# Performance work log

Hardware: AMD Instinct MI355X
Metric: run time of the kernel (lower is better)

The kernel has to match this reference:

```python
import jax, jax.numpy as jnp
import numpy as np

B, S, D, H, NB = 512, 200, 256, 4, 2
DH = D // H
N_ITEMS = 100001  # item_num + 1 (padding idx 0)
EPS = 1e-8


def _ln(x, g, b):
    m = x.mean(-1, keepdims=True)
    v = ((x - m) ** 2).mean(-1, keepdims=True)
    return (x - m) / jnp.sqrt(v + EPS) * g + b


def setup_inputs() -> dict:
    key = jax.random.key(0)
    ks = jax.random.split(key, 20)
    f32 = jnp.float32
    item_emb = jax.random.normal(ks[0], (N_ITEMS, D), f32) * 0.02
    item_emb = item_emb.at[0].set(0.0)  # padding_idx=0
    pos_emb = jax.random.normal(ks[1], (S, D), f32) * 0.02
    inp = {
        'item_emb': item_emb,
        'pos_emb': pos_emb,
        'ln1_g': jnp.ones((NB, D), f32),
        'ln1_b': jnp.zeros((NB, D), f32),
        'in_w': jax.random.normal(ks[2], (NB, 3 * D, D), f32) * 0.02,
        'in_b': jnp.zeros((NB, 3 * D), f32),
        'out_w': jax.random.normal(ks[3], (NB, D, D), f32) * 0.02,
        'out_b': jnp.zeros((NB, D), f32),
        'ln2_g': jnp.ones((NB, D), f32),
        'ln2_b': jnp.zeros((NB, D), f32),
        'c1_w': jax.random.normal(ks[4], (NB, D, D), f32) * 0.02,
        'c1_b': jnp.zeros((NB, D), f32),
        'c2_w': jax.random.normal(ks[5], (NB, D, D), f32) * 0.02,
        'c2_b': jnp.zeros((NB, D), f32),
        'last_g': jnp.ones((D,), f32),
        'last_b': jnp.zeros((D,), f32),
        'user_ids': jax.random.randint(ks[6], (B,), 0, 10000),
        'log_seqs': jax.random.randint(ks[7], (B, S), 0, N_ITEMS),
        'pos_seqs': jax.random.randint(ks[8], (B, S), 0, N_ITEMS),
        'neg_seqs': jax.random.randint(ks[9], (B, S), 0, N_ITEMS),
    }
    return inp


def reference(item_emb, pos_emb, ln1_g, ln1_b, in_w, in_b, out_w, out_b,
              ln2_g, ln2_b, c1_w, c1_b, c2_w, c2_b, last_g, last_b,
              user_ids, log_seqs, pos_seqs, neg_seqs):
    seqs = item_emb[log_seqs] * jnp.asarray(D ** 0.5, item_emb.dtype)
    seqs = seqs + pos_emb[None, :, :]  # positions = arange(S)
    tl_mask = (log_seqs != 0)[..., None].astype(seqs.dtype)  # [B,S,1]
    seqs = seqs * tl_mask
    causal = jnp.tril(jnp.ones((S, S), bool))  # True = attend
    scale = 1.0 / np.sqrt(DH)
    for i in range(NB):
        Q = _ln(seqs, ln1_g[i], ln1_b[i])
        q = (Q @ in_w[i, :D].T + in_b[i, :D]).reshape(B, S, H, DH)
        k = (seqs @ in_w[i, D:2 * D].T + in_b[i, D:2 * D]).reshape(B, S, H, DH)
        v = (seqs @ in_w[i, 2 * D:].T + in_b[i, 2 * D:]).reshape(B, S, H, DH)
        scores = jnp.einsum('bqhd,bkhd->bhqk', q, k) * scale
        scores = jnp.where(causal[None, None], scores, -jnp.inf)
        attn = jax.nn.softmax(scores, axis=-1)
        o = jnp.einsum('bhqk,bkhd->bqhd', attn, v).reshape(B, S, D)
        o = o @ out_w[i].T + out_b[i]
        seqs = Q + o  # residual is on layernormed Q (as in source)
        seqs = _ln(seqs, ln2_g[i], ln2_b[i])
        h1 = jax.nn.relu(seqs @ c1_w[i].T + c1_b[i])
        seqs = (h1 @ c2_w[i].T + c2_b[i] + seqs) * tl_mask
    log_feats = _ln(seqs, last_g, last_b)
    pos_embs = item_emb[pos_seqs]
    neg_embs = item_emb[neg_seqs]
    pos_logits = (log_feats * pos_embs).sum(-1)
    neg_logits = (log_feats * neg_embs).sum(-1)
    return (pos_logits, neg_logits)
```

## Files before the change

### kernel.cpp

```cpp
#include <hip/hip_runtime.h>
#include <math.h>

namespace {

constexpr int kB = 512, kS = 200, kD = 256, kH = 4;
constexpr int kM = kB * kS;
constexpr float kEps = 1e-8f;

typedef short bf16x8 __attribute__((ext_vector_type(8)));
typedef float f32x4 __attribute__((ext_vector_type(4)));

__device__ __forceinline__ float bf2f(unsigned short s) {
  return __uint_as_float(((unsigned)s) << 16);
}
__device__ __forceinline__ unsigned cvtpk(float lo, float hi) {
  unsigned r;
  asm("v_cvt_pk_bf16_f32 %0, %1, %2" : "=v"(r) : "v"(lo), "v"(hi));
  return r;
}
__device__ __forceinline__ void gload16(const void* g, void* l) {
  __builtin_amdgcn_global_load_lds(
      (const __attribute__((address_space(1))) void*)g,
      (__attribute__((address_space(3))) void*)l, 16, 0, 0);
}
__device__ __forceinline__ void vm3() { asm volatile("s_waitcnt vmcnt(3)" ::: "memory"); }
__device__ __forceinline__ void vm0() { asm volatile("s_waitcnt vmcnt(0)" ::: "memory"); }
__device__ __forceinline__ void lk0() { asm volatile("s_waitcnt lgkmcnt(0)" ::: "memory"); }
__device__ __forceinline__ void bar() { asm volatile("s_barrier" ::: "memory"); }

__global__ __launch_bounds__(256) void cvt4_kernel(
    const float* __restrict__ w0, const float* __restrict__ w1,
    const float* __restrict__ w2, const float* __restrict__ w3,
    const float* __restrict__ ln1g,
    unsigned short* __restrict__ o0, unsigned short* __restrict__ o1,
    unsigned short* __restrict__ o2, unsigned short* __restrict__ o3) {
  int blk = blockIdx.x;
  const float* src;
  unsigned short* dst;
  int base;
  bool isin = false;
  if (blk < 384)      { src = w0; dst = o0; base = blk; isin = true; }
  else if (blk < 512) { src = w1; dst = o1; base = blk - 384; }
  else if (blk < 640) { src = w2; dst = o2; base = blk - 512; }
  else                { src = w3; dst = o3; base = blk - 640; }
  int i4 = (base * 256 + threadIdx.x) * 4;
  float4 v = *reinterpret_cast<const float4*>(src + i4);
  if (isin) {
    int layer = (i4 >= 196608) ? 1 : 0;
    int rem = i4 - layer * 196608;
    int n = rem >> 8;
    int k = rem & 255;
    if (n < 256) {
      float4 g = *reinterpret_cast<const float4*>(ln1g + layer * 256 + k);
      v.x *= g.x; v.y *= g.y; v.z *= g.z; v.w *= g.w;
    }
  }
  uint2 o = {cvtpk(v.x, v.y), cvtpk(v.z, v.w)};
  *reinterpret_cast<uint2*>(dst + i4) = o;
}

__global__ __launch_bounds__(64) void s1s2_kernel(
    const float* __restrict__ in_w, const float* __restrict__ in_b,
    const float* __restrict__ ln1g, const float* __restrict__ ln1b,
    float* __restrict__ s1o, float* __restrict__ s2o) {
  int blk = blockIdx.x;
  int layer = blk >> 8, n = blk & 255;
  int k = threadIdx.x * 4;
  float4 w = *reinterpret_cast<const float4*>(in_w + (size_t)layer * 196608 + n * 256 + k);
  float4 g = *reinterpret_cast<const float4*>(ln1g + layer * 256 + k);
  float4 b = *reinterpret_cast<const float4*>(ln1b + layer * 256 + k);
  float a = w.x * g.x + w.y * g.y + w.z * g.z + w.w * g.w;
  float c = w.x * b.x + w.y * b.y + w.z * b.z + w.w * b.w;
#pragma unroll
  for (int o = 32; o >= 1; o >>= 1) { a += __shfl_xor(a, o); c += __shfl_xor(c, o); }
  if (threadIdx.x == 0) {
    s1o[blk] = a;
    s2o[blk] = c + in_b[layer * 768 + n];
  }
}

__global__ __launch_bounds__(512) void embed_kernel(
    const float* __restrict__ item_emb, const float* __restrict__ pos_emb,
    const int* __restrict__ log_seqs, unsigned short* __restrict__ x,
    float2* __restrict__ stats) {
  int bs = blockIdx.x * 8 + (threadIdx.x >> 6);
  int s = bs % kS;
  int idx = log_seqs[bs];
  float msk = (idx != 0) ? 1.f : 0.f;
  int t = threadIdx.x & 63;
  float4 a = reinterpret_cast<const float4*>(item_emb + (size_t)idx * kD)[t];
  float4 p = reinterpret_cast<const float4*>(pos_emb + (size_t)s * kD)[t];
  float v[4];
  v[0] = (a.x * 16.f + p.x) * msk;
  v[1] = (a.y * 16.f + p.y) * msk;
  v[2] = (a.z * 16.f + p.z) * msk;
  v[3] = (a.w * 16.f + p.w) * msk;
  uint2 r = {cvtpk(v[0], v[1]), cvtpk(v[2], v[3])};
  reinterpret_cast<uint2*>(x + (size_t)bs * kD)[t] = r;
  float sm = v[0] + v[1] + v[2] + v[3];
#pragma unroll
  for (int o = 32; o >= 1; o >>= 1) sm += __shfl_xor(sm, o);
  float mean = sm * (1.f / kD);
  float d0 = v[0] - mean, d1 = v[1] - mean, d2 = v[2] - mean, d3 = v[3] - mean;
  float vs = d0 * d0 + d1 * d1 + d2 * d2 + d3 * d3;
#pragma unroll
  for (int o = 32; o >= 1; o >>= 1) vs += __shfl_xor(vs, o);
  if (t == 0) stats[bs] = {mean, rsqrtf(vs * (1.f / kD) + kEps)};
}

template <int MODE, int LN, int G3>
__global__ __launch_bounds__(512, 4) void gemm2(
    const unsigned short* __restrict__ A, int lda,
    const unsigned short* __restrict__ W,
    const float* __restrict__ bias,
    const unsigned short* __restrict__ R, int ldr,
    const int* __restrict__ logseq,
    const float* __restrict__ lng, const float* __restrict__ lnb,
    const float* __restrict__ qg, const float* __restrict__ qb,
    const float2* __restrict__ statsIn, float2* __restrict__ statsOut,
    const float* __restrict__ s1v, const float* __restrict__ s2v,
    const float* __restrict__ iembf, const int* __restrict__ posq,
    const int* __restrict__ negq, float* __restrict__ outlg,
    unsigned short* __restrict__ C, int ldc) {
  __shared__ __attribute__((aligned(16))) unsigned short SMEM[36864];
  __shared__ float red1[128][4];
  __shared__ float red2[128][4];
  const int tid = threadIdx.x, lane = tid & 63, wid = tid >> 6;
  int m0, n0;
  if (G3) {
    int g = blockIdx.x / 24, sub = blockIdx.x % 24;
    m0 = (g * 8 + (sub & 7)) * 128;
    n0 = (sub >> 3) * 256;
  } else {
    m0 = blockIdx.x * 128;
    n0 = 0;
  }
  const int wm = wid >> 2, wn = wid & 3;
  const int lrow = lane & 15, kgrp = lane >> 4;
  const int srow = tid >> 2;
  const int sslot = (tid & 3) ^ (srow & 3);
  const unsigned short* gA  = A + (size_t)(m0 + srow) * lda + sslot * 8;
  const unsigned short* gW0 = W + (size_t)(n0 + srow) * kD + sslot * 8;
  const unsigned short* gW1 = gW0 + (size_t)128 * kD;
  const int sa = (kgrp ^ (lrow & 3)) * 8;

#define STAGE(kk, bb)                                                   \
  do {                                                                  \
    gload16(gA + (kk) * 32, &SMEM[(bb) * 4096 + wid * 512]);            \
    gload16(gW0 + (kk) * 32, &SMEM[12288 + (bb) * 8192 + wid * 512]);   \
    gload16(gW1 + (kk) * 32, &SMEM[16384 + (bb) * 8192 + wid * 512]);   \
  } while (0)

  f32x4 acc[4][4] = {};
  STAGE(0, 0);
  STAGE(1, 1);
#pragma unroll
  for (int k = 0; k < 8; ++k) {
    if (k < 7) vm3(); else vm0();
    bar();
    const int buf = k % 3;
    bf16x8 af[4], bfr[4];
#pragma unroll
    for (int x = 0; x < 4; ++x) {
      af[x]  = *reinterpret_cast<const bf16x8*>(
          &SMEM[12288 + buf * 8192 + (wn * 64 + x * 16 + lrow) * 32 + sa]);
      bfr[x] = *reinterpret_cast<const bf16x8*>(
          &SMEM[buf * 4096 + (wm * 64 + x * 16 + lrow) * 32 + sa]);
    }
    if (k + 2 < 8) STAGE(k + 2, (k + 2) % 3);
    __builtin_amdgcn_s_setprio(1);
#pragma unroll
    for (int na = 0; na < 4; ++na)
#pragma unroll
      for (int mb = 0; mb < 4; ++mb)
        acc[na][mb] = __builtin_amdgcn_mfma_f32_16x16x32_bf16(
            af[na], bfr[mb], acc[na][mb], 0, 0, 0);
    __builtin_amdgcn_s_setprio(0);
  }
#undef STAGE
  __syncthreads();
  const bool qpath = (MODE == 4) && (n0 == 0);
  float msk[4];
  float2 st[4];
  if (MODE == 3 || MODE == 6) {
#pragma unroll
    for (int mb = 0; mb < 4; ++mb)
      msk[mb] = (logseq[m0 + wm * 64 + mb * 16 + lrow] != 0) ? 1.f : 0.f;
  }
  if (MODE == 5 || (MODE == 4 && n0 == 0)) {
#pragma unroll
    for (int mb = 0; mb < 4; ++mb)
      st[mb] = statsIn[m0 + wm * 64 + mb * 16 + lrow];
  }

  auto computeX = [&](int na, int mb, float x[4]) {
    const int gcol = n0 + wn * 64 + na * 16 + kgrp * 4;
    const f32x4 v = acc[na][mb];
    if (MODE == 4 && qpath) {
      float4 t1 = *reinterpret_cast<const float4*>(s1v + gcol);
      float4 t2 = *reinterpret_cast<const float4*>(s2v + gcol);
      const float s1f[4] = {t1.x, t1.y, t1.z, t1.w};
      const float s2f[4] = {t2.x, t2.y, t2.z, t2.w};
#pragma unroll
      for (int r = 0; r < 4; ++r)
        x[r] = st[mb].y * (v[r] - st[mb].x * s1f[r]) + s2f[r];
      return;
    }
    float4 b4 = *reinterpret_cast<const float4*>(bias + gcol);
    const float bx[4] = {b4.x, b4.y, b4.z, b4.w};
    if (MODE == 1) {
#pragma unroll
      for (int r = 0; r < 4; ++r) x[r] = fmaxf(v[r] + bx[r], 0.f);
    } else if (MODE == 4) {
#pragma unroll
      for (int r = 0; r < 4; ++r) x[r] = v[r] + bx[r];
    } else if (MODE == 3 || MODE == 6) {
      int m = m0 + wm * 64 + mb * 16 + lrow;
      ushort4 rv = *reinterpret_cast<const ushort4*>(R + (size_t)m * ldr + gcol);
      const unsigned short* rs = reinterpret_cast<const unsigned short*>(&rv);
#pragma unroll
      for (int r = 0; r < 4; ++r)
        x[r] = (v[r] + bx[r] + bf2f(rs[r])) * msk[mb];
    } else {
      int m = m0 + wm * 64 + mb * 16 + lrow;
      ushort4 rv = *reinterpret_cast<const ushort4*>(R + (size_t)m * ldr + gcol);
      const unsigned short* rs = reinterpret_cast<const unsigned short*>(&rv);
      float4 t1 = *reinterpret_cast<const float4*>(qg + gcol);
      float4 t2 = *reinterpret_cast<const float4*>(qb + gcol);
      const float g4[4] = {t1.x, t1.y, t1.z, t1.w};
      const float qb4[4] = {t2.x, t2.y, t2.z, t2.w};
#pragma unroll
      for (int r = 0; r < 4; ++r) {
        float q = (bf2f(rs[r]) - st[mb].x) * st[mb].y * g4[r] + qb4[r];
        x[r] = v[r] + bx[r] + q;
      }
    }
  };

  if (MODE == 6) {
    float* SL = reinterpret_cast<float*>(SMEM);
    int pi[4], ni[4];
#pragma unroll
    for (int mb = 0; mb < 4; ++mb) {
      int m = m0 + wm * 64 + mb * 16 + lrow;
      pi[mb] = posq[m];
      ni[mb] = negq[m];
    }
#pragma unroll
    for (int mb = 0; mb < 4; ++mb) {
      float4 peL[4], neL[4];
#pragma unroll
      for (int na = 0; na < 4; ++na) {
        int gcol = n0 + wn * 64 + na * 16 + kgrp * 4;
        peL[na] = *reinterpret_cast<const float4*>(iembf + (size_t)pi[mb] * 256 + gcol);
        neL[na] = *reinterpret_cast<const float4*>(iembf + (size_t)ni[mb] * 256 + gcol);
      }
      float sa_ = 0.f, sb_ = 0.f;
      float s1p = 0.f, s2p = 0.f, s3p = 0.f;
      float s1n = 0.f, s2n = 0.f, s3n = 0.f;
#pragma unroll
      for (int na = 0; na < 4; ++na) {
        float x[4];
        computeX(na, mb, x);
        int gcol = n0 + wn * 64 + na * 16 + kgrp * 4;
        float4 g4v = *reinterpret_cast<const float4*>(lng + gcol);
        float4 b4v = *reinterpret_cast<const float4*>(lnb + gcol);
        const float gg[4] = {g4v.x, g4v.y, g4v.z, g4v.w};
        const float lb[4] = {b4v.x, b4v.y, b4v.z, b4v.w};
        const float pef[4] = {peL[na].x, peL[na].y, peL[na].z, peL[na].w};
        const float nef[4] = {neL[na].x, neL[na].y, neL[na].z, neL[na].w};
#pragma unroll
        for (int r = 0; r < 4; ++r) {
          sa_ += x[r];
          sb_ += x[r] * x[r];
          float gp = gg[r] * pef[r], gn = gg[r] * nef[r];
          s1p += x[r] * gp; s2p += gp; s3p += lb[r] * pef[r];
          s1n += x[r] * gn; s2n += gn; s3n += lb[r] * nef[r];
        }
      }
      float vals[8] = {sa_, sb_, s1p, s2p, s3p, s1n, s2n, s3n};
#pragma unroll
      for (int j = 0; j < 8; ++j) {
        vals[j] += __shfl_xor(vals[j], 16);
        vals[j] += __shfl_xor(vals[j], 32);
      }
      if (kgrp == 0) {
        int rl = wm * 64 + mb * 16 + lrow;
        float* dst = &SL[rl * 33 + wn * 8];
#pragma unroll
        for (int j = 0; j < 8; ++j) dst[j] = vals[j];
      }
    }
    __syncthreads();
    if (tid < 128) {
      float t[8] = {0.f, 0.f, 0.f, 0.f, 0.f, 0.f, 0.f, 0.f};
#pragma unroll
      for (int w = 0; w < 4; ++w) {
        const float* src = &SL[tid * 33 + w * 8];
#pragma unroll
        for (int j = 0; j < 8; ++j) t[j] += src[j];
      }
      float mean = t[0] * (1.f / 256.f);
      float var = t[1] * (1.f / 256.f) - mean * mean;
      float inv = rsqrtf(fmaxf(var, 0.f) + kEps);
      int m = m0 + tid;
      outlg[m] = inv * (t[2] - mean * t[3]) + t[4];
      outlg[(size_t)kM + m] = inv * (t[5] - mean * t[6]) + t[7];
    }
    return;
  }

  float mean[4], inv[4];
  if (LN) {
    float sA[4] = {0.f, 0.f, 0.f, 0.f}, sB[4] = {0.f, 0.f, 0.f, 0.f};
#pragma unroll
    for (int na = 0; na < 4; ++na)
#pragma unroll
      for (int mb = 0; mb < 4; ++mb) {
        float x[4];
        computeX(na, mb, x);
#pragma unroll
        for (int r = 0; r < 4; ++r) { sA[mb] += x[r]; sB[mb] += x[r] * x[r]; }
      }
#pragma unroll
    for (int mb = 0; mb < 4; ++mb) {
      sA[mb] += __shfl_xor(sA[mb], 16); sA[mb] += __shfl_xor(sA[mb], 32);
      sB[mb] += __shfl_xor(sB[mb], 16); sB[mb] += __shfl_xor(sB[mb], 32);
    }
    if (kgrp == 0) {
#pragma unroll
      for (int mb = 0; mb < 4; ++mb) {
        int rl = wm * 64 + mb * 16 + lrow;
        red1[rl][wn] = sA[mb];
        red2[rl][wn] = sB[mb];
      }
    }
    __syncthreads();
#pragma unroll
    for (int mb = 0; mb < 4; ++mb) {
      int rl = wm * 64 + mb * 16 + lrow;
      float4 p1 = *reinterpret_cast<const float4*>(red1[rl]);
      float4 p2 = *reinterpret_cast<const float4*>(red2[rl]);
      float t1 = p1.x + p1.y + p1.z + p1.w;
      float t2 = p2.x + p2.y + p2.z + p2.w;
      float mu = t1 * (1.f / 256.f);
      float var = t2 * (1.f / 256.f) - mu * mu;
      mean[mb] = mu;
      inv[mb] = rsqrtf(fmaxf(var, 0.f) + kEps);
    }
    if (LN == 3 && wn == 0 && kgrp == 0) {
#pragma unroll
      for (int mb = 0; mb < 4; ++mb)
        statsOut[m0 + wm * 64 + mb * 16 + lrow] = {mean[mb], inv[mb]};
    }
  }

  unsigned short* eb = &SMEM[wid * 3072];
  const int rr = lane >> 2, c8 = (lane & 3) * 8;
#pragma unroll
  for (int hh = 0; hh < 2; ++hh) {
    lk0();
#pragma unroll
    for (int mbl = 0; mbl < 2; ++mbl) {
      int mb = hh * 2 + mbl;
#pragma unroll
      for (int na = 0; na < 4; ++na) {
        float x[4];
        computeX(na, mb, x);
        if (LN == 1) {
          int gcol = n0 + wn * 64 + na * 16 + kgrp * 4;
          float4 g4v = *reinterpret_cast<const float4*>(lng + gcol);
          float4 b4v = *reinterpret_cast<const float4*>(lnb + gcol);
          x[0] = (x[0] - mean[mb]) * inv[mb] * g4v.x + b4v.x;
          x[1] = (x[1] - mean[mb]) * inv[mb] * g4v.y + b4v.y;
          x[2] = (x[2] - mean[mb]) * inv[mb] * g4v.z + b4v.z;
          x[3] = (x[3] - mean[mb]) * inv[mb] * g4v.w + b4v.w;
        }
        uint2 o = {cvtpk(x[0], x[1]), cvtpk(x[2], x[3])};
        *reinterpret_cast<uint2*>(&eb[(mbl * 16 + lrow) * 72 + na * 16 + kgrp * 4]) = o;
      }
    }
    lk0();
#pragma unroll
    for (int rh = 0; rh < 2; ++rh) {
      int row = rh * 16 + rr;
      uint4 d0 = *reinterpret_cast<const uint4*>(&eb[row * 72 + c8]);
      uint4 d1 = *reinterpret_cast<const uint4*>(&eb[row * 72 + 32 + c8]);
      size_t gbase = (size_t)(m0 + wm * 64 + hh * 32 + row) * ldc + (n0 + wn * 64 + c8);
      *reinterpret_cast<uint4*>(C + gbase) = d0;
      *reinterpret_cast<uint4*>(C + gbase + 32) = d1;
    }
  }
}

__global__ __launch_bounds__(512) void attn_mfma(unsigned short* __restrict__ qkv) {
  constexpr int kVS = 232, kQS = 768;
  __shared__ __attribute__((aligned(16))) unsigned short Kl[200 * 64];
  __shared__ __attribute__((aligned(16))) unsigned short Vt[64 * kVS];
  __shared__ __attribute__((aligned(16))) unsigned short Pt[8 * 636];
  int b = blockIdx.x >> 2, h = blockIdx.x & 3;
  int tid = threadIdx.x, lane = tid & 63, wid = tid >> 6;
  const unsigned short* kvb = qkv + (size_t)b * kS * kQS + 256 + h * 64;
  for (int i = tid; i < 1600; i += 512) {
    int row = i >> 3, slot = i & 7;
    *reinterpret_cast<uint4*>(&Kl[row * 64 + ((slot ^ (row & 7)) << 3)]) =
        *reinterpret_cast<const uint4*>(kvb + (size_t)row * kQS + slot * 8);
  }
  for (int i = tid; i < 3200; i += 512) {
    int row = i >> 4, d0 = (i & 15) * 4;
    ushort4 v = *reinterpret_cast<const ushort4*>(kvb + 256 + (size_t)row * kQS + d0);
    Vt[(d0 + 0) * kVS + row] = v.x;
    Vt[(d0 + 1) * kVS + row] = v.y;
    Vt[(d0 + 2) * kVS + row] = v.z;
    Vt[(d0 + 3) * kVS + row] = v.w;
  }
  for (int i = tid; i < 2048; i += 512) {
    int d = i >> 5, c = i & 31;
    Vt[d * kVS + 200 + c] = 0;
  }
  __syncthreads();

  int qcol = lane & 15, kgrp = lane >> 4;
  const float scale2 = 0.18033688f;
  int packed = (wid < 3) ? (0xFFFC - wid) : (0xFF09 + (wid - 3) * 15);
  unsigned short* ptw = &Pt[wid * 636];
#pragma unroll
  for (int ti = 0; ti < 2; ++ti) {
    int t = (packed >> (ti * 4)) & 15;
    if (t == 15) break;
    int qb = t * 16;
    int qrow = qb + qcol;
    int qm = min(qrow, kS - 1);
    const unsigned short* qrp = qkv + (size_t)(b * kS + qm) * kQS + h * 64;
    bf16x8 qf0 = *reinterpret_cast<const bf16x8*>(qrp + kgrp * 8);
    bf16x8 qf1 = *reinterpret_cast<const bf16x8*>(qrp + 32 + kgrp * 8);
    f32x4 accO[4] = {};
    float l_run = 0.f;
    int nc = (qb + 47) >> 5;
    for (int c = 0; c < nc; ++c) {
      int kbase = c * 32;
      f32x4 s0 = {}, s1 = {};
      int kr0 = min(kbase + qcol, kS - 1);
      int kr1 = min(kbase + 16 + qcol, kS - 1);
      const unsigned short* K0a = &Kl[kr0 * 64 + ((kgrp ^ (kr0 & 7)) << 3)];
      const unsigned short* K0b = &Kl[kr0 * 64 + (((kgrp + 4) ^ (kr0 & 7)) << 3)];
      const unsigned short* K1a = &Kl[kr1 * 64 + ((kgrp ^ (kr1 & 7)) << 3)];
      const unsigned short* K1b = &Kl[kr1 * 64 + (((kgrp + 4) ^ (kr1 & 7)) << 3)];
      s0 = __builtin_amdgcn_mfma_f32_16x16x32_bf16(*reinterpret_cast<const bf16x8*>(K0a), qf0, s0, 0, 0, 0);
      s0 = __builtin_amdgcn_mfma_f32_16x16x32_bf16(*reinterpret_cast<const bf16x8*>(K0b), qf1, s0, 0, 0, 0);
      s1 = __builtin_amdgcn_mfma_f32_16x16x32_bf16(*reinterpret_cast<const bf16x8*>(K1a), qf0, s1, 0, 0, 0);
      s1 = __builtin_amdgcn_mfma_f32_16x16x32_bf16(*reinterpret_cast<const bf16x8*>(K1b), qf1, s1, 0, 0, 0);
      float p[8];
      float psum = 0.f;
#pragma unroll
      for (int r = 0; r < 4; ++r) {
        int key0 = kbase + kgrp * 4 + r;
        int key1 = key0 + 16;
        float x0 = (key0 <= qm) ? fmaf(s0[r], scale2, -8.f) : -3.0e38f;
        float x1 = (key1 <= qm) ? fmaf(s1[r], scale2, -8.f) : -3.0e38f;
        p[r] = exp2f(x0);
        p[r + 4] = exp2f(x1);
        psum += p[r] + p[r + 4];
      }
      l_run += psum;
      uint2 w0 = {cvtpk(p[0], p[1]), cvtpk(p[2], p[3])};
      uint2 w1 = {cvtpk(p[4], p[5]), cvtpk(p[6], p[7])};
      *reinterpret_cast<uint2*>(&ptw[qcol * 40 + kgrp * 4]) = w0;
      *reinterpret_cast<uint2*>(&ptw[qcol * 40 + 16 + kgrp * 4]) = w1;
      bf16x8 pf = *reinterpret_cast<const bf16x8*>(&ptw[qcol * 40 + kgrp * 8]);
#pragma unroll
      for (int nf = 0; nf < 4; ++nf) {
        bf16x8 vf = *reinterpret_cast<const bf16x8*>(
            &Vt[(nf * 16 + qcol) * kVS + kbase + kgrp * 8]);
        accO[nf] = __builtin_amdgcn_mfma_f32_16x16x32_bf16(vf, pf, accO[nf], 0, 0, 0);
      }
    }
    float l_tot = l_run;
    l_tot += __shfl_xor(l_tot, 16);
    l_tot += __shfl_xor(l_tot, 32);
    float inv = 1.f / l_tot;
    if (qrow < kS) {
      unsigned short* op = qkv + (size_t)(b * kS + qrow) * kQS + h * 64;
#pragma unroll
      for (int nf = 0; nf < 4; ++nf) {
        uint2 o4 = {cvtpk(accO[nf][0] * inv, accO[nf][1] * inv),
                    cvtpk(accO[nf][2] * inv, accO[nf][3] * inv)};
        *reinterpret_cast<uint2*>(op + nf * 16 + kgrp * 4) = o4;
      }
    }
  }
}

}

extern "C" void kernel_launch(void* const* d_in, const int* in_sizes, int n_in,
                              void* d_out, int out_size, void* d_ws,
                              size_t ws_size, hipStream_t stream) {
  const float* item_emb = (const float*)d_in[0];
  const float* pos_emb  = (const float*)d_in[1];
  const float* ln1_g = (const float*)d_in[2];
  const float* ln1_b = (const float*)d_in[3];
  const float* in_w  = (const float*)d_in[4];
  const float* in_b  = (const float*)d_in[5];
  const float* out_w = (const float*)d_in[6];
  const float* out_b = (const float*)d_in[7];
  const float* ln2_g = (const float*)d_in[8];
  const float* ln2_b = (const float*)d_in[9];
  const float* c1_w  = (const float*)d_in[10];
  const float* c1_b  = (const float*)d_in[11];
  const float* c2_w  = (const float*)d_in[12];
  const float* c2_b  = (const float*)d_in[13];
  const float* last_g = (const float*)d_in[14];
  const float* last_b = (const float*)d_in[15];
  const int* log_seqs = (const int*)d_in[17];
  const int* pos_seqs = (const int*)d_in[18];
  const int* neg_seqs = (const int*)d_in[19];
  float* out = (float*)d_out;

  size_t unit = (size_t)kM * kD;
  unsigned short* X   = (unsigned short*)d_ws;
  unsigned short* QKV = X + unit;
  unsigned short* inw_bf  = X + 4 * unit;
  unsigned short* outw_bf = inw_bf + 2 * 768 * 256;
  unsigned short* c1w_bf  = outw_bf + 2 * 256 * 256;
  unsigned short* c2w_bf  = c1w_bf + 2 * 256 * 256;
  float2* stats = (float2*)(c2w_bf + 2 * 256 * 256);
  float* s1buf = (float*)(stats + 2 * kM);
  float* s2buf = s1buf + 512;

  cvt4_kernel<<<768, 256, 0, stream>>>(in_w, out_w, c1_w, c2_w, ln1_g,
                                       inw_bf, outw_bf, c1w_bf, c2w_bf);
  s1s2_kernel<<<512, 64, 0, stream>>>(in_w, in_b, ln1_g, ln1_b, s1buf, s2buf);
  embed_kernel<<<kM / 8, 512, 0, stream>>>(item_emb, pos_emb, log_seqs, X, stats);

  dim3 g1(kM / 128, 1);
  for (int l = 0; l < 2; ++l) {
    const unsigned short* iw = inw_bf + (size_t)l * 768 * 256;
    float2* stl = stats + (size_t)l * kM;
    gemm2<4, 0, 1><<<kM / 128 * 3, 512, 0, stream>>>(
        X, 256, iw, in_b + l * 768, nullptr, 0, nullptr,
        nullptr, nullptr, nullptr, nullptr, stl, nullptr,
        s1buf + l * 256, s2buf + l * 256, nullptr, nullptr, nullptr, nullptr,
        QKV, 768);
    attn_mfma<<<kB * kH, 512, 0, stream>>>(QKV);
    gemm2<5, 1, 0><<<g1, 512, 0, stream>>>(
        QKV, 768, outw_bf + (size_t)l * kD * kD, out_b + l * kD, X, 256, nullptr,
        ln2_g + l * kD, ln2_b + l * kD, ln1_g + l * kD, ln1_b + l * kD,
        stl, nullptr, nullptr, nullptr, nullptr, nullptr, nullptr, nullptr,
        QKV + 256, 768);
    gemm2<1, 0, 0><<<g1, 512, 0, stream>>>(
        QKV + 256, 768, c1w_bf + (size_t)l * kD * kD, c1_b + l * kD, nullptr, 0,
        nullptr, nullptr, nullptr, nullptr, nullptr, nullptr, nullptr,
        nullptr, nullptr, nullptr, nullptr, nullptr, nullptr, QKV + 512, 768);
    if (l == 0) {
      gemm2<3, 3, 0><<<g1, 512, 0, stream>>>(
          QKV + 512, 768, c2w_bf, c2_b, QKV + 256, 768, log_seqs,
          nullptr, nullptr, nullptr, nullptr, nullptr, stats + kM,
          nullptr, nullptr, nullptr, nullptr, nullptr, nullptr, X, 256);
    } else {
      gemm2<6, 0, 0><<<g1, 512, 0, stream>>>(
          QKV + 512, 768, c2w_bf + (size_t)kD * kD, c2_b + kD, QKV + 256, 768,
          log_seqs, last_g, last_b, nullptr, nullptr, nullptr, nullptr,
          nullptr, nullptr, item_emb, pos_seqs, neg_seqs, out, X, 256);
    }
  }
}
```

Before: 658.9 us.

## Fuse FFN c1 and c2 GEMMs into one kernel keeping hidden in LDS

Replaces the separate c1 (ReLU) GEMM and c2 residual/LN-stats or final-logit GEMM with a single ffn_fused kernel using 64-row tiles. The ReLU hidden activations stay in swizzled shared memory instead of round-tripping through global QKV storage. The kernel double-buffers weight loads, and the epilogues for layer 0 (stats out) and layer 1 (logits) move into it. Smaller tiles and two weight sweeps per block add weight traffic and may lower MFMA efficiency per block.

```diff
diff --git a/kernel.cpp b/kernel.cpp
--- a/kernel.cpp
+++ b/kernel.cpp
@@ -24,6 +24,7 @@
       (__attribute__((address_space(3))) void*)l, 16, 0, 0);
 }
 __device__ __forceinline__ void vm3() { asm volatile("s_waitcnt vmcnt(3)" ::: "memory"); }
+__device__ __forceinline__ void vm2() { asm volatile("s_waitcnt vmcnt(2)" ::: "memory"); }
 __device__ __forceinline__ void vm0() { asm volatile("s_waitcnt vmcnt(0)" ::: "memory"); }
 __device__ __forceinline__ void lk0() { asm volatile("s_waitcnt lgkmcnt(0)" ::: "memory"); }
 __device__ __forceinline__ void bar() { asm volatile("s_barrier" ::: "memory"); }
@@ -114,13 +115,10 @@
     const unsigned short* __restrict__ W,
     const float* __restrict__ bias,
     const unsigned short* __restrict__ R, int ldr,
-    const int* __restrict__ logseq,
     const float* __restrict__ lng, const float* __restrict__ lnb,
     const float* __restrict__ qg, const float* __restrict__ qb,
-    const float2* __restrict__ statsIn, float2* __restrict__ statsOut,
+    const float2* __restrict__ statsIn,
     const float* __restrict__ s1v, const float* __restrict__ s2v,
-    const float* __restrict__ iembf, const int* __restrict__ posq,
-    const int* __restrict__ negq, float* __restrict__ outlg,
     unsigned short* __restrict__ C, int ldc) {
   __shared__ __attribute__((aligned(16))) unsigned short SMEM[36864];
   __shared__ float red1[128][4];
@@ -180,13 +178,7 @@
 #undef STAGE
   __syncthreads();
   const bool qpath = (MODE == 4) && (n0 == 0);
-  float msk[4];
   float2 st[4];
-  if (MODE == 3 || MODE == 6) {
-#pragma unroll
-    for (int mb = 0; mb < 4; ++mb)
-      msk[mb] = (logseq[m0 + wm * 64 + mb * 16 + lrow] != 0) ? 1.f : 0.f;
-  }
   if (MODE == 5 || (MODE == 4 && n0 == 0)) {
 #pragma unroll
     for (int mb = 0; mb < 4; ++mb)
@@ -208,19 +200,9 @@
     }
     float4 b4 = *reinterpret_cast<const float4*>(bias + gcol);
     const float bx[4] = {b4.x, b4.y, b4.z, b4.w};
-    if (MODE == 1) {
-#pragma unroll
-      for (int r = 0; r < 4; ++r) x[r] = fmaxf(v[r] + bx[r], 0.f);
-    } else if (MODE == 4) {
+    if (MODE == 4) {
 #pragma unroll
       for (int r = 0; r < 4; ++r) x[r] = v[r] + bx[r];
-    } else if (MODE == 3 || MODE == 6) {
-      int m = m0 + wm * 64 + mb * 16 + lrow;
-      ushort4 rv = *reinterpret_cast<const ushort4*>(R + (size_t)m * ldr + gcol);
-      const unsigned short* rs = reinterpret_cast<const unsigned short*>(&rv);
-#pragma unroll
-      for (int r = 0; r < 4; ++r)
-        x[r] = (v[r] + bx[r] + bf2f(rs[r])) * msk[mb];
     } else {
       int m = m0 + wm * 64 + mb * 16 + lrow;
       ushort4 rv = *reinterpret_cast<const ushort4*>(R + (size_t)m * ldr + gcol);
@@ -236,79 +218,6 @@
       }
     }
   };
-
-  if (MODE == 6) {
-    float* SL = reinterpret_cast<float*>(SMEM);
-    int pi[4], ni[4];
-#pragma unroll
-    for (int mb = 0; mb < 4; ++mb) {
-      int m = m0 + wm * 64 + mb * 16 + lrow;
-      pi[mb] = posq[m];
-      ni[mb] = negq[m];
-    }
-#pragma unroll
-    for (int mb = 0; mb < 4; ++mb) {
-      float4 peL[4], neL[4];
-#pragma unroll
-      for (int na = 0; na < 4; ++na) {
-        int gcol = n0 + wn * 64 + na * 16 + kgrp * 4;
-        peL[na] = *reinterpret_cast<const float4*>(iembf + (size_t)pi[mb] * 256 + gcol);
-        neL[na] = *reinterpret_cast<const float4*>(iembf + (size_t)ni[mb] * 256 + gcol);
-      }
-      float sa_ = 0.f, sb_ = 0.f;
-      float s1p = 0.f, s2p = 0.f, s3p = 0.f;
-      float s1n = 0.f, s2n = 0.f, s3n = 0.f;
-#pragma unroll
-      for (int na = 0; na < 4; ++na) {
-        float x[4];
-        computeX(na, mb, x);
-        int gcol = n0 + wn * 64 + na * 16 + kgrp * 4;
-        float4 g4v = *reinterpret_cast<const float4*>(lng + gcol);
-        float4 b4v = *reinterpret_cast<const float4*>(lnb + gcol);
-        const float gg[4] = {g4v.x, g4v.y, g4v.z, g4v.w};
-        const float lb[4] = {b4v.x, b4v.y, b4v.z, b4v.w};
-        const float pef[4] = {peL[na].x, peL[na].y, peL[na].z, peL[na].w};
-        const float nef[4] = {neL[na].x, neL[na].y, neL[na].z, neL[na].w};
-#pragma unroll
-        for (int r = 0; r < 4; ++r) {
-          sa_ += x[r];
-          sb_ += x[r] * x[r];
-          float gp = gg[r] * pef[r], gn = gg[r] * nef[r];
-          s1p += x[r] * gp; s2p += gp; s3p += lb[r] * pef[r];
-          s1n += x[r] * gn; s2n += gn; s3n += lb[r] * nef[r];
-        }
-      }
-      float vals[8] = {sa_, sb_, s1p, s2p, s3p, s1n, s2n, s3n};
-#pragma unroll
-      for (int j = 0; j < 8; ++j) {
-        vals[j] += __shfl_xor(vals[j], 16);
-        vals[j] += __shfl_xor(vals[j], 32);
-      }
-      if (kgrp == 0) {
-        int rl = wm * 64 + mb * 16 + lrow;
-        float* dst = &SL[rl * 33 + wn * 8];
-#pragma unroll
-        for (int j = 0; j < 8; ++j) dst[j] = vals[j];
-      }
-    }
-    __syncthreads();
-    if (tid < 128) {
-      float t[8] = {0.f, 0.f, 0.f, 0.f, 0.f, 0.f, 0.f, 0.f};
-#pragma unroll
-      for (int w = 0; w < 4; ++w) {
-        const float* src = &SL[tid * 33 + w * 8];
-#pragma unroll
-        for (int j = 0; j < 8; ++j) t[j] += src[j];
-      }
-      float mean = t[0] * (1.f / 256.f);
-      float var = t[1] * (1.f / 256.f) - mean * mean;
-      float inv = rsqrtf(fmaxf(var, 0.f) + kEps);
-      int m = m0 + tid;
-      outlg[m] = inv * (t[2] - mean * t[3]) + t[4];
-      outlg[(size_t)kM + m] = inv * (t[5] - mean * t[6]) + t[7];
-    }
-    return;
-  }
 
   float mean[4], inv[4];
   if (LN) {
@@ -347,11 +256,6 @@
       float var = t2 * (1.f / 256.f) - mu * mu;
       mean[mb] = mu;
       inv[mb] = rsqrtf(fmaxf(var, 0.f) + kEps);
-    }
-    if (LN == 3 && wn == 0 && kgrp == 0) {
-#pragma unroll
-      for (int mb = 0; mb < 4; ++mb)
-        statsOut[m0 + wm * 64 + mb * 16 + lrow] = {mean[mb], inv[mb]};
     }
   }
 
@@ -390,6 +294,285 @@
       *reinterpret_cast<uint4*>(C + gbase) = d0;
       *reinterpret_cast<uint4*>(C + gbase + 32) = d1;
     }
+  }
+}
+
+template <int LAST>
+__global__ __launch_bounds__(512, 4) void ffn_fused(
+    const unsigned short* __restrict__ A, int lda,
+    const unsigned short* __restrict__ W1, const float* __restrict__ b1,
+    const unsigned short* __restrict__ W2, const float* __restrict__ b2,
+    const int* __restrict__ logseq,
+    const float* __restrict__ lng, const float* __restrict__ lnb,
+    float2* __restrict__ statsOut,
+    const float* __restrict__ iembf, const int* __restrict__ posq,
+    const int* __restrict__ negq, float* __restrict__ outlg,
+    unsigned short* __restrict__ C, int ldc) {
+  __shared__ __attribute__((aligned(16))) unsigned short SMEM[36864];
+  __shared__ float red1[64][4];
+  __shared__ float red2[64][4];
+  const int tid = threadIdx.x, lane = tid & 63, wid = tid >> 6;
+  const int m0 = blockIdx.x * 64;
+  const int wm = wid >> 2, wn = wid & 3;
+  const int lrow = lane & 15, kgrp = lane >> 4;
+  unsigned short* As = SMEM;
+  unsigned short* Ws = SMEM + 4096;
+  unsigned short* H1 = SMEM + 20480;
+  const int arow = (wid & 3) * 16 + (lane >> 2);
+  const int aslot = (lane & 3) ^ (arow & 3);
+  const unsigned short* gA = A + (size_t)(m0 + arow) * lda + aslot * 8;
+  const int wrow0 = wid * 32 + (lane >> 2);
+  const int wrow1 = wrow0 + 16;
+  const int ws0 = (lane & 3) ^ (wrow0 & 3);
+  const int ws1 = (lane & 3) ^ (wrow1 & 3);
+  const unsigned short* gW10 = W1 + wrow0 * 256 + ws0 * 8;
+  const unsigned short* gW11 = W1 + wrow1 * 256 + ws1 * 8;
+  const unsigned short* gW20 = W2 + wrow0 * 256 + ws0 * 8;
+  const unsigned short* gW21 = W2 + wrow1 * 256 + ws1 * 8;
+  const int sa = (kgrp ^ (lrow & 3)) * 8;
+  const f32x4 zero = {0.f, 0.f, 0.f, 0.f};
+
+#define STG1(kk, bb)                                               \
+  do {                                                             \
+    if (wid < 4) gload16(gA + (kk) * 32, &As[(bb) * 2048 + wid * 512]); \
+    gload16(gW10 + (kk) * 32, &Ws[(bb) * 8192 + wid * 1024]);      \
+    gload16(gW11 + (kk) * 32, &Ws[(bb) * 8192 + wid * 1024 + 512]);\
+  } while (0)
+
+  f32x4 acc[4][2] = {};
+  STG1(0, 0);
+  STG1(1, 1);
+#pragma unroll
+  for (int k = 0; k < 8; ++k) {
+    if (k < 7) { if (wid < 4) vm3(); else vm2(); } else vm0();
+    bar();
+    const int buf = k & 1;
+    bf16x8 af[4], bfr[2];
+#pragma unroll
+    for (int x = 0; x < 4; ++x)
+      af[x] = *reinterpret_cast<const bf16x8*>(
+          &Ws[buf * 8192 + (wn * 64 + x * 16 + lrow) * 32 + sa]);
+#pragma unroll
+    for (int mb = 0; mb < 2; ++mb)
+      bfr[mb] = *reinterpret_cast<const bf16x8*>(
+          &As[buf * 2048 + (wm * 32 + mb * 16 + lrow) * 32 + sa]);
+    __builtin_amdgcn_s_setprio(1);
+#pragma unroll
+    for (int na = 0; na < 4; ++na)
+#pragma unroll
+      for (int mb = 0; mb < 2; ++mb)
+        acc[na][mb] = __builtin_amdgcn_mfma_f32_16x16x32_bf16(
+            af[na], bfr[mb], acc[na][mb], 0, 0, 0);
+    __builtin_amdgcn_s_setprio(0);
+    bar();
+    if (k + 2 < 8) STG1(k + 2, k & 1);
+  }
+#undef STG1
+#pragma unroll
+  for (int na = 0; na < 4; ++na) {
+    int c0 = wn * 64 + na * 16 + kgrp * 4;
+    float4 b4 = *reinterpret_cast<const float4*>(b1 + c0);
+#pragma unroll
+    for (int mb = 0; mb < 2; ++mb) {
+      int row = wm * 32 + mb * 16 + lrow;
+      f32x4 v = acc[na][mb];
+      float x0 = fmaxf(v[0] + b4.x, 0.f), x1 = fmaxf(v[1] + b4.y, 0.f);
+      float x2 = fmaxf(v[2] + b4.z, 0.f), x3 = fmaxf(v[3] + b4.w, 0.f);
+      int s = wn * 8 + na * 2 + (kgrp >> 1);
+      int addr = row * 256 + ((s ^ (row & 7)) << 3) + (kgrp & 1) * 4;
+      uint2 o = {cvtpk(x0, x1), cvtpk(x2, x3)};
+      *reinterpret_cast<uint2*>(&H1[addr]) = o;
+    }
+  }
+  __syncthreads();
+#pragma unroll
+  for (int na = 0; na < 4; ++na)
+#pragma unroll
+    for (int mb = 0; mb < 2; ++mb) acc[na][mb] = zero;
+
+#define STG2(kk, bb)                                               \
+  do {                                                             \
+    gload16(gW20 + (kk) * 32, &Ws[(bb) * 8192 + wid * 1024]);      \
+    gload16(gW21 + (kk) * 32, &Ws[(bb) * 8192 + wid * 1024 + 512]);\
+  } while (0)
+
+  STG2(0, 0);
+  STG2(1, 1);
+#pragma unroll
+  for (int k = 0; k < 8; ++k) {
+    if (k < 7) vm2(); else vm0();
+    bar();
+    const int buf = k & 1;
+    bf16x8 af[4], bfr[2];
+#pragma unroll
+    for (int x = 0; x < 4; ++x)
+      af[x] = *reinterpret_cast<const bf16x8*>(
+          &Ws[buf * 8192 + (wn * 64 + x * 16 + lrow) * 32 + sa]);
+#pragma unroll
+    for (int mb = 0; mb < 2; ++mb) {
+      int row = wm * 32 + mb * 16 + lrow;
+      bfr[mb] = *reinterpret_cast<const bf16x8*>(
+          &H1[row * 256 + (((k * 4 + kgrp) ^ (row & 7)) << 3)]);
+    }
+    __builtin_amdgcn_s_setprio(1);
+#pragma unroll
+    for (int na = 0; na < 4; ++na)
+#pragma unroll
+      for (int mb = 0; mb < 2; ++mb)
+        acc[na][mb] = __builtin_amdgcn_mfma_f32_16x16x32_bf16(
+            af[na], bfr[mb], acc[na][mb], 0, 0, 0);
+    __builtin_amdgcn_s_setprio(0);
+    bar();
+    if (k + 2 < 8) STG2(k + 2, k & 1);
+  }
+#undef STG2
+  __syncthreads();
+
+  float msk[2];
+#pragma unroll
+  for (int mb = 0; mb < 2; ++mb)
+    msk[mb] = (logseq[m0 + wm * 32 + mb * 16 + lrow] != 0) ? 1.f : 0.f;
+
+  auto computeY = [&](int na, int mb, float x[4]) {
+    int gcol = wn * 64 + na * 16 + kgrp * 4;
+    int m = m0 + wm * 32 + mb * 16 + lrow;
+    f32x4 v = acc[na][mb];
+    float4 b4 = *reinterpret_cast<const float4*>(b2 + gcol);
+    ushort4 rv = *reinterpret_cast<const ushort4*>(A + (size_t)m * lda + gcol);
+    const unsigned short* rs = reinterpret_cast<const unsigned short*>(&rv);
+    const float bx[4] = {b4.x, b4.y, b4.z, b4.w};
+#pragma unroll
+    for (int r = 0; r < 4; ++r)
+      x[r] = (v[r] + bx[r] + bf2f(rs[r])) * msk[mb];
+  };
+
+  if (LAST == 0) {
+    float sA[2] = {0.f, 0.f}, sB[2] = {0.f, 0.f};
+#pragma unroll
+    for (int na = 0; na < 4; ++na)
+#pragma unroll
+      for (int mb = 0; mb < 2; ++mb) {
+        float x[4];
+        computeY(na, mb, x);
+#pragma unroll
+        for (int r = 0; r < 4; ++r) { sA[mb] += x[r]; sB[mb] += x[r] * x[r]; }
+      }
+#pragma unroll
+    for (int mb = 0; mb < 2; ++mb) {
+      sA[mb] += __shfl_xor(sA[mb], 16); sA[mb] += __shfl_xor(sA[mb], 32);
+      sB[mb] += __shfl_xor(sB[mb], 16); sB[mb] += __shfl_xor(sB[mb], 32);
+    }
+    if (kgrp == 0) {
+#pragma unroll
+      for (int mb = 0; mb < 2; ++mb) {
+        int rl = wm * 32 + mb * 16 + lrow;
+        red1[rl][wn] = sA[mb];
+        red2[rl][wn] = sB[mb];
+      }
+    }
+    __syncthreads();
+    if (wn == 0 && kgrp == 0) {
+#pragma unroll
+      for (int mb = 0; mb < 2; ++mb) {
+        int rl = wm * 32 + mb * 16 + lrow;
+        float4 p1 = *reinterpret_cast<const float4*>(red1[rl]);
+        float4 p2 = *reinterpret_cast<const float4*>(red2[rl]);
+        float t1 = p1.x + p1.y + p1.z + p1.w;
+        float t2 = p2.x + p2.y + p2.z + p2.w;
+        float mu = t1 * (1.f / 256.f);
+        float var = t2 * (1.f / 256.f) - mu * mu;
+        statsOut[m0 + rl] = {mu, rsqrtf(fmaxf(var, 0.f) + kEps)};
+      }
+    }
+    unsigned short* eb = &SMEM[wid * 2560];
+#pragma unroll
+    for (int mb = 0; mb < 2; ++mb)
+#pragma unroll
+      for (int na = 0; na < 4; ++na) {
+        float x[4];
+        computeY(na, mb, x);
+        uint2 o = {cvtpk(x[0], x[1]), cvtpk(x[2], x[3])};
+        *reinterpret_cast<uint2*>(&eb[(mb * 16 + lrow) * 72 + na * 16 + kgrp * 4]) = o;
+      }
+    lk0();
+#pragma unroll
+    for (int rh = 0; rh < 4; ++rh) {
+      int row = rh * 8 + (lane >> 3);
+      uint4 d = *reinterpret_cast<const uint4*>(&eb[row * 72 + (lane & 7) * 8]);
+      *reinterpret_cast<uint4*>(
+          C + (size_t)(m0 + wm * 32 + row) * ldc + wn * 64 + (lane & 7) * 8) = d;
+    }
+    return;
+  }
+
+  float* SL = reinterpret_cast<float*>(SMEM);
+  int pi[2], ni[2];
+#pragma unroll
+  for (int mb = 0; mb < 2; ++mb) {
+    int m = m0 + wm * 32 + mb * 16 + lrow;
+    pi[mb] = posq[m];
+    ni[mb] = negq[m];
+  }
+#pragma unroll
+  for (int mb = 0; mb < 2; ++mb) {
+    float4 peL[4], neL[4];
+#pragma unroll
+    for (int na = 0; na < 4; ++na) {
+      int gcol = wn * 64 + na * 16 + kgrp * 4;
+      peL[na] = *reinterpret_cast<const float4*>(iembf + (size_t)pi[mb] * 256 + gcol);
+      neL[na] = *reinterpret_cast<const float4*>(iembf + (size_t)ni[mb] * 256 + gcol);
+    }
+    float sa_ = 0.f, sb_ = 0.f;
+    float s1p = 0.f, s2p = 0.f, s3p = 0.f;
+    float s1n = 0.f, s2n = 0.f, s3n = 0.f;
+#pragma unroll
+    for (int na = 0; na < 4; ++na) {
+      float x[4];
+      computeY(na, mb, x);
+      int gcol = wn * 64 + na * 16 + kgrp * 4;
+      float4 g4v = *reinterpret_cast<const float4*>(lng + gcol);
+      float4 b4v = *reinterpret_cast<const float4*>(lnb + gcol);
+      const float gg[4] = {g4v.x, g4v.y, g4v.z, g4v.w};
+      const float lb[4] = {b4v.x, b4v.y, b4v.z, b4v.w};
+      const float pef[4] = {peL[na].x, peL[na].y, peL[na].z, peL[na].w};
+      const float nef[4] = {neL[na].x, neL[na].y, neL[na].z, neL[na].w};
+#pragma unroll
+      for (int r = 0; r < 4; ++r) {
+        sa_ += x[r];
+        sb_ += x[r] * x[r];
+        float gp = gg[r] * pef[r], gn = gg[r] * nef[r];
+        s1p += x[r] * gp; s2p += gp; s3p += lb[r] * pef[r];
+        s1n += x[r] * gn; s2n += gn; s3n += lb[r] * nef[r];
+      }
+    }
+    float vals[8] = {sa_, sb_, s1p, s2p, s3p, s1n, s2n, s3n};
+#pragma unroll
+    for (int j = 0; j < 8; ++j) {
+      vals[j] += __shfl_xor(vals[j], 16);
+      vals[j] += __shfl_xor(vals[j], 32);
+    }
+    if (kgrp == 0) {
+      int rl = wm * 32 + mb * 16 + lrow;
+      float* dst = &SL[rl * 33 + wn * 8];
+#pragma unroll
+      for (int j = 0; j < 8; ++j) dst[j] = vals[j];
+    }
+  }
+  __syncthreads();
+  if (tid < 64) {
+    float t[8] = {0.f, 0.f, 0.f, 0.f, 0.f, 0.f, 0.f, 0.f};
+#pragma unroll
+    for (int w = 0; w < 4; ++w) {
+      const float* src = &SL[tid * 33 + w * 8];
+#pragma unroll
+      for (int j = 0; j < 8; ++j) t[j] += src[j];
+    }
+    float mean = t[0] * (1.f / 256.f);
+    float var = t[1] * (1.f / 256.f) - mean * mean;
+    float inv = rsqrtf(fmaxf(var, 0.f) + kEps);
+    int m = m0 + tid;
+    outlg[m] = inv * (t[2] - mean * t[3]) + t[4];
+    outlg[(size_t)kM + m] = inv * (t[5] - mean * t[6]) + t[7];
   }
 }
 
@@ -538,30 +721,24 @@
     const unsigned short* iw = inw_bf + (size_t)l * 768 * 256;
     float2* stl = stats + (size_t)l * kM;
     gemm2<4, 0, 1><<<kM / 128 * 3, 512, 0, stream>>>(
-        X, 256, iw, in_b + l * 768, nullptr, 0, nullptr,
-        nullptr, nullptr, nullptr, nullptr, stl, nullptr,
-        s1buf + l * 256, s2buf + l * 256, nullptr, nullptr, nullptr, nullptr,
-        QKV, 768);
+        X, 256, iw, in_b + l * 768, nullptr, 0,
+        nullptr, nullptr, nullptr, nullptr, stl,
+        s1buf + l * 256, s2buf + l * 256, QKV, 768);
     attn_mfma<<<kB * kH, 512, 0, stream>>>(QKV);
     gemm2<5, 1, 0><<<g1, 512, 0, stream>>>(
-        QKV, 768, outw_bf + (size_t)l * kD * kD, out_b + l * kD, X, 256, nullptr,
+        QKV, 768, outw_bf + (size_t)l * kD * kD, out_b + l * kD, X, 256,
         ln2_g + l * kD, ln2_b + l * kD, ln1_g + l * kD, ln1_b + l * kD,
-        stl, nullptr, nullptr, nullptr, nullptr, nullptr, nullptr, nullptr,
-        QKV + 256, 768);
-    gemm2<1, 0, 0><<<g1, 512, 0, stream>>>(
-        QKV + 256, 768, c1w_bf + (size_t)l * kD * kD, c1_b + l * kD, nullptr, 0,
-        nullptr, nullptr, nullptr, nullptr, nullptr, nullptr, nullptr,
-        nullptr, nullptr, nullptr, nullptr, nullptr, nullptr, QKV + 512, 768);
+        stl, nullptr, nullptr, QKV + 256, 768);
     if (l == 0) {
-      gemm2<3, 3, 0><<<g1, 512, 0, stream>>>(
-          QKV + 512, 768, c2w_bf, c2_b, QKV + 256, 768, log_seqs,
-          nullptr, nullptr, nullptr, nullptr, nullptr, stats + kM,
-          nullptr, nullptr, nullptr, nullptr, nullptr, nullptr, X, 256);
+      ffn_fused<0><<<kM / 64, 512, 0, stream>>>(
+          QKV + 256, 768, c1w_bf, c1_b, c2w_bf, c2_b, log_seqs,
+          nullptr, nullptr, stats + kM, nullptr, nullptr, nullptr, nullptr,
+          X, 256);
     } else {
-      gemm2<6, 0, 0><<<g1, 512, 0, stream>>>(
-          QKV + 512, 768, c2w_bf + (size_t)kD * kD, c2_b + kD, QKV + 256, 768,
-          log_seqs, last_g, last_b, nullptr, nullptr, nullptr, nullptr,
-          nullptr, nullptr, item_emb, pos_seqs, neg_seqs, out, X, 256);
-    }
-  }
-}
+      ffn_fused<1><<<kM / 64, 512, 0, stream>>>(
+          QKV + 256, 768, c1w_bf + 65536, c1_b + 256, c2w_bf + 65536, c2_b + 256,
+          log_seqs, last_g, last_b, nullptr, item_emb, pos_seqs, neg_seqs, out,
+          nullptr, 0);
+    }
+  }
+}
```

Measured after the change: 612.6 us. 7.0% less time.
